# Kernel optimization log

Measured on AMD Instinct MI355X. Metric: run time of the kernel, lower is better.

## Reference

```python
import jax, jax.numpy as jnp
import numpy as np

N_NODES = 120000  # n_entities + n_users
N_REL = 16
D = 64   # entity_dim
R = 64   # relation_dim
E = 1600000


def setup_inputs() -> dict:
    key = jax.random.key(0)
    k1, k2, k3, k4, k5, k6 = jax.random.split(key, 6)
    return {
        "entity_user_embed": jax.random.normal(k1, (N_NODES, D), dtype=jnp.float32) * 0.1,
        "relation_embed": jax.random.normal(k2, (N_REL, R), dtype=jnp.float32) * 0.1,
        "W_R": jax.random.normal(k3, (N_REL, D, R), dtype=jnp.float32) * 0.1,
        "edge_src": jax.random.randint(k4, (E,), 0, N_NODES, dtype=jnp.int32),
        "edge_dst": jax.random.randint(k5, (E,), 0, N_NODES, dtype=jnp.int32),
        "edge_type": jax.random.randint(k6, (E,), 0, N_REL, dtype=jnp.int32),
    }


def reference(entity_user_embed, relation_embed, W_R, edge_src, edge_dst, edge_type):
    n_nodes = entity_user_embed.shape[0]
    # Per-relation transform of every node embedding: [n_rel, n_nodes, R].
    # Equivalent to the per-relation edge loop: matmul(emb[id], W_R[r]).
    trans = jnp.einsum('nd,rdk->rnk', entity_user_embed, W_R)
    r_mul_t = trans[edge_type, edge_src]   # [E, R] (edges.src path)
    r_mul_h = trans[edge_type, edge_dst]   # [E, R] (edges.dst path)
    r_embed = relation_embed[edge_type]    # [E, R]
    # bmm([E,1,R], [E,R,1]) -> per-edge dot product
    att = jnp.sum(r_mul_t * jnp.tanh(r_mul_h + r_embed), axis=-1)  # [E]
    # edge softmax over incoming edges of each destination node
    att_max = jax.ops.segment_max(att, edge_dst, num_segments=n_nodes)
    ex = jnp.exp(att - att_max[edge_dst])
    denom = jax.ops.segment_sum(ex, edge_dst, num_segments=n_nodes)
    out = ex / denom[edge_dst]
    return out[:, None]  # [E, 1], matching squeeze(-1) of [E,1,1]
```

## Files before the change

kernel.cpp:

```cpp
#include <hip/hip_runtime.h>
#include <hip/hip_bf16.h>

#define D64 64
#define NREL 16
#define SCALE 32.0f
#define INV_SCALE 0.03125f

typedef __attribute__((ext_vector_type(8))) short bf16x8;
typedef __attribute__((ext_vector_type(4))) float f32x4;
typedef __attribute__((ext_vector_type(2))) float f32x2;

__device__ __forceinline__ float tanh_fast(float x) {
    float e = __expf(2.0f * x);
    return 1.0f - 2.0f / (e + 1.0f);
}

__device__ __forceinline__ float tanh_poly(float x) {
    x = fmaxf(-1.5f, fminf(1.5f, x));
    float u = x * x;
    float p = fmaf(u, -0.0182227f, 0.108952f);
    p = fmaf(u, p, -0.329139f);
    p = fmaf(u, p, 1.0f);
    return x * p;
}

__device__ __forceinline__ unsigned short f2b(float x) {
    __hip_bfloat16 h = __float2bfloat16(x);
    return *reinterpret_cast<unsigned short*>(&h);
}

__global__ void prep_kernel(const float* __restrict__ WR, const float* __restrict__ rel,
                            unsigned short* __restrict__ Wt, float* __restrict__ relp,
                            float* __restrict__ denom, int n_nodes) {
    int i = blockIdx.x * blockDim.x + threadIdx.x;
    if (i < NREL * D64 * D64) {
        int r = i >> 12, rem = i & 4095, c = rem >> 6, d = rem & 63;
        Wt[i] = f2b(WR[(r << 12) + (d << 6) + c] * SCALE);
    }
    if (i < NREL * D64) {
        int t = i >> 6, kp = i & 63;
        int q = kp >> 4, m = (kp >> 2) & 3, g = kp & 3;
        relp[i] = rel[t * D64 + m * 16 + q * 4 + g];
    }
    if (i < n_nodes) denom[i] = 0.0f;
}

__global__ __launch_bounds__(256)
void trans_gemm_kernel(const float* __restrict__ emb,
                       const unsigned short* __restrict__ Wt,
                       uint4* __restrict__ trans,
                       int n_nodes) {
    __shared__ unsigned short lbuf[8 * 4096];
    const int tid  = threadIdx.x;
    const int lane = tid & 63;
    const int wid  = tid >> 6;
    const int col  = lane & 15;
    const int quad = lane >> 4;
    const int rbase = (blockIdx.x & 1) * 8;
    const int nodebase = (blockIdx.x >> 1) * 256 + wid * 64;

    const unsigned short* wbase = Wt + (rbase << 12);
    #pragma unroll
    for (int k = 0; k < 16; ++k) {
        int c = tid + k * 256;
        int rr = c >> 9, cc = c & 511;
        int mt = cc >> 7, q2 = (cc >> 6) & 1, ln = cc & 63;
        int so = (rr << 12) + ((mt * 16 + (ln & 15)) << 6) + (q2 << 5) + ((ln >> 4) << 3);
        *(bf16x8*)(&lbuf[c << 3]) = *(const bf16x8*)(wbase + so);
    }

    bf16x8 bfr[4][2];
    int nds[4];
    #pragma unroll
    for (int j = 0; j < 4; ++j) {
        int node = nodebase + j * 16 + col;
        nds[j] = node;
        int cn = node < n_nodes ? node : n_nodes - 1;
        const float* bp = emb + (size_t)cn * D64 + quad * 8;
        #pragma unroll
        for (int ks = 0; ks < 2; ++ks) {
            float4 v0 = *(const float4*)(bp + ks * 32);
            float4 v1 = *(const float4*)(bp + ks * 32 + 4);
            bfr[j][ks][0] = (short)f2b(v0.x); bfr[j][ks][1] = (short)f2b(v0.y);
            bfr[j][ks][2] = (short)f2b(v0.z); bfr[j][ks][3] = (short)f2b(v0.w);
            bfr[j][ks][4] = (short)f2b(v1.x); bfr[j][ks][5] = (short)f2b(v1.y);
            bfr[j][ks][6] = (short)f2b(v1.z); bfr[j][ks][7] = (short)f2b(v1.w);
        }
    }

    __syncthreads();

    #pragma unroll 1
    for (int rr = 0; rr < 8; ++rr) {
        const int r = rbase + rr;
        const unsigned short* lb = lbuf + (rr << 12);
        f32x4 acc[4][4];
        #pragma unroll
        for (int mt = 0; mt < 4; ++mt) {
            bf16x8 a0 = *(const bf16x8*)(lb + (mt << 10) + (lane << 3));
            bf16x8 a1 = *(const bf16x8*)(lb + (mt << 10) + 512 + (lane << 3));
            #pragma unroll
            for (int j = 0; j < 4; ++j) {
                f32x4 c = {0.f, 0.f, 0.f, 0.f};
                c = __builtin_amdgcn_mfma_f32_16x16x32_bf16(a0, bfr[j][0], c, 0, 0, 0);
                c = __builtin_amdgcn_mfma_f32_16x16x32_bf16(a1, bfr[j][1], c, 0, 0, 0);
                acc[mt][j] = c;
            }
        }
        #pragma unroll
        for (int j = 0; j < 4; ++j) {
            if (nds[j] < n_nodes) {
                uint4 pk;
                unsigned p;
                p = __builtin_amdgcn_cvt_pk_fp8_f32(acc[0][j][0], acc[0][j][1], 0, false);
                p = __builtin_amdgcn_cvt_pk_fp8_f32(acc[0][j][2], acc[0][j][3], p, true);
                pk.x = p;
                p = __builtin_amdgcn_cvt_pk_fp8_f32(acc[1][j][0], acc[1][j][1], 0, false);
                p = __builtin_amdgcn_cvt_pk_fp8_f32(acc[1][j][2], acc[1][j][3], p, true);
                pk.y = p;
                p = __builtin_amdgcn_cvt_pk_fp8_f32(acc[2][j][0], acc[2][j][1], 0, false);
                p = __builtin_amdgcn_cvt_pk_fp8_f32(acc[2][j][2], acc[2][j][3], p, true);
                pk.z = p;
                p = __builtin_amdgcn_cvt_pk_fp8_f32(acc[3][j][0], acc[3][j][1], 0, false);
                p = __builtin_amdgcn_cvt_pk_fp8_f32(acc[3][j][2], acc[3][j][3], p, true);
                pk.w = p;
                trans[((size_t)r * n_nodes + nds[j]) * 4 + quad] = pk;
            }
        }
    }
}

__device__ __forceinline__ void term4(unsigned ut, unsigned uh, float4 r, float& acc) {
    f32x2 tlo = __builtin_amdgcn_cvt_pk_f32_fp8(ut, false);
    f32x2 thi = __builtin_amdgcn_cvt_pk_f32_fp8(ut, true);
    f32x2 hlo = __builtin_amdgcn_cvt_pk_f32_fp8(uh, false);
    f32x2 hhi = __builtin_amdgcn_cvt_pk_f32_fp8(uh, true);
    acc += tlo[0] * tanh_poly(fmaf(hlo[0], INV_SCALE, r.x));
    acc += tlo[1] * tanh_poly(fmaf(hlo[1], INV_SCALE, r.y));
    acc += thi[0] * tanh_poly(fmaf(hhi[0], INV_SCALE, r.z));
    acc += thi[1] * tanh_poly(fmaf(hhi[1], INV_SCALE, r.w));
}

__global__ __launch_bounds__(256)
void edge_kernel(const unsigned* __restrict__ trans,
                 const float* __restrict__ relp,
                 const int* __restrict__ esrc, const int* __restrict__ edst,
                 const int* __restrict__ etype,
                 float* __restrict__ out, float* __restrict__ denom,
                 int E, int n_nodes) {
    int e0 = blockIdx.x * 512 + threadIdx.x;
    int e1 = e0 + 256;
    bool v0 = e0 < E, v1 = e1 < E;
    int i0 = v0 ? e0 : 0;
    int i1 = v1 ? e1 : 0;
    int t0 = etype[i0], s0 = esrc[i0], d0 = edst[i0];
    int t1 = etype[i1], s1 = esrc[i1], d1 = edst[i1];

    const uint4* pt0 = (const uint4*)(trans + ((size_t)t0 * n_nodes + s0) * 16);
    const uint4* ph0 = (const uint4*)(trans + ((size_t)t0 * n_nodes + d0) * 16);
    const uint4* pt1 = (const uint4*)(trans + ((size_t)t1 * n_nodes + s1) * 16);
    const uint4* ph1 = (const uint4*)(trans + ((size_t)t1 * n_nodes + d1) * 16);

    uint4 T0[4], H0[4], T1[4], H1[4];
    #pragma unroll
    for (int c4 = 0; c4 < 4; ++c4) {
        T0[c4] = pt0[c4]; H0[c4] = ph0[c4];
        T1[c4] = pt1[c4]; H1[c4] = ph1[c4];
    }

    const float4* pr0 = (const float4*)(relp + t0 * D64);
    const float4* pr1 = (const float4*)(relp + t1 * D64);
    float a0 = 0.f, a1 = 0.f;
    #pragma unroll
    for (int c4 = 0; c4 < 4; ++c4) {
        term4(T0[c4].x, H0[c4].x, pr0[c4 * 4 + 0], a0);
        term4(T1[c4].x, H1[c4].x, pr1[c4 * 4 + 0], a1);
        term4(T0[c4].y, H0[c4].y, pr0[c4 * 4 + 1], a0);
        term4(T1[c4].y, H1[c4].y, pr1[c4 * 4 + 1], a1);
        term4(T0[c4].z, H0[c4].z, pr0[c4 * 4 + 2], a0);
        term4(T1[c4].z, H1[c4].z, pr1[c4 * 4 + 2], a1);
        term4(T0[c4].w, H0[c4].w, pr0[c4 * 4 + 3], a0);
        term4(T1[c4].w, H1[c4].w, pr1[c4 * 4 + 3], a1);
    }
    if (v0) {
        float ex = __expf(a0 * INV_SCALE);
        out[e0] = ex;
        atomicAdd(&denom[d0], ex);
    }
    if (v1) {
        float ex = __expf(a1 * INV_SCALE);
        out[e1] = ex;
        atomicAdd(&denom[d1], ex);
    }
}

__global__ void normalize_kernel(float* __restrict__ out,
                                 const float* __restrict__ denom,
                                 const int* __restrict__ edst, int E) {
    int e = blockIdx.x * blockDim.x + threadIdx.x;
    if (e < E) out[e] = out[e] / denom[edst[e]];
}

__global__ void zero_denom_kernel(float* __restrict__ denom, int n) {
    int i = blockIdx.x * blockDim.x + threadIdx.x;
    if (i < n) denom[i] = 0.0f;
}

__global__ __launch_bounds__(256)
void edge_att_fallback(const float* __restrict__ emb, const float* __restrict__ rel,
                       const float* __restrict__ WR, const int* __restrict__ esrc,
                       const int* __restrict__ edst, const int* __restrict__ etype,
                       float* __restrict__ exbuf, float* __restrict__ denom,
                       int E, int chunkSize) {
    const int type = blockIdx.x & 15;
    const int c    = blockIdx.x >> 4;
    const int lane = threadIdx.x & 63;
    const int wid  = threadIdx.x >> 6;
    long base0 = (long)c * (long)chunkSize;
    long cend  = base0 + chunkSize;
    if (cend > E) cend = E;
    if (base0 >= cend) return;
    int per = (chunkSize + 3) >> 2;
    long wbeg = base0 + (long)wid * per;
    long wend = wbeg + per;
    if (wend > cend) wend = cend;
    if (wbeg >= wend) return;
    float w[D64];
    const float* Wt = WR + (size_t)type * D64 * D64;
    #pragma unroll
    for (int d = 0; d < D64; ++d) w[d] = Wt[d * D64 + lane];
    const float rk = rel[type * D64 + lane];
    for (long s0 = wbeg; s0 < wend; s0 += 64) {
        long e = s0 + lane;
        int ty = -1, sv = 0, dv = 0;
        if (e < wend) { ty = etype[e]; sv = esrc[e]; dv = edst[e]; }
        unsigned long long m = __ballot(ty == type);
        while (m) {
            int b = __builtin_ctzll(m);
            m &= m - 1;
            int sn = __builtin_amdgcn_readlane(sv, b);
            int dn = __builtin_amdgcn_readlane(dv, b);
            const float4* es4 = (const float4*)(emb + (size_t)sn * D64);
            const float4* ed4 = (const float4*)(emb + (size_t)dn * D64);
            float t0 = 0.f, t1 = 0.f, t2 = 0.f, t3 = 0.f;
            float h0 = 0.f, h1 = 0.f, h2 = 0.f, h3 = 0.f;
            #pragma unroll
            for (int i = 0; i < D64 / 4; ++i) {
                float4 a = es4[i]; float4 b4 = ed4[i];
                t0 = fmaf(a.x, w[4*i+0], t0); t1 = fmaf(a.y, w[4*i+1], t1);
                t2 = fmaf(a.z, w[4*i+2], t2); t3 = fmaf(a.w, w[4*i+3], t3);
                h0 = fmaf(b4.x, w[4*i+0], h0); h1 = fmaf(b4.y, w[4*i+1], h1);
                h2 = fmaf(b4.z, w[4*i+2], h2); h3 = fmaf(b4.w, w[4*i+3], h3);
            }
            float t = (t0 + t1) + (t2 + t3);
            float h = (h0 + h1) + (h2 + h3);
            float p = t * tanh_fast(h + rk);
            #pragma unroll
            for (int off = 32; off > 0; off >>= 1) p += __shfl_xor(p, off);
            if (lane == 0) {
                float ex = __expf(p);
                exbuf[s0 + b] = ex;
                atomicAdd(&denom[dn], ex);
            }
        }
    }
}

__global__ void normalize_fallback(float* __restrict__ out,
                                   const float* __restrict__ denom,
                                   const int* __restrict__ edst, int E) {
    int e = blockIdx.x * blockDim.x + threadIdx.x;
    if (e < E) out[e] = out[e] / denom[edst[e]];
}

extern "C" void kernel_launch(void* const* d_in, const int* in_sizes, int n_in,
                              void* d_out, int out_size, void* d_ws, size_t ws_size,
                              hipStream_t stream) {
    const float* emb  = (const float*)d_in[0];
    const float* rel  = (const float*)d_in[1];
    const float* WR   = (const float*)d_in[2];
    const int*   esrc = (const int*)d_in[3];
    const int*   edst = (const int*)d_in[4];
    const int*   ety  = (const int*)d_in[5];

    const int E       = in_sizes[3];
    const int n_nodes = in_sizes[0] / D64;
    float* out = (float*)d_out;

    size_t transB = (size_t)NREL * n_nodes * D64;
    size_t off_trans = 0;
    size_t off_wt    = (off_trans + transB + 255) & ~(size_t)255;
    size_t off_rel   = (off_wt + (size_t)NREL * D64 * D64 * 2 + 255) & ~(size_t)255;
    size_t off_den   = (off_rel + (size_t)NREL * D64 * 4 + 255) & ~(size_t)255;
    size_t need      = off_den + (size_t)n_nodes * sizeof(float);

    if (ws_size >= need) {
        uint4*          trans = (uint4*)((char*)d_ws + off_trans);
        unsigned short* Wt    = (unsigned short*)((char*)d_ws + off_wt);
        float*          relp  = (float*)((char*)d_ws + off_rel);
        float*          denom = (float*)((char*)d_ws + off_den);

        int prepN = n_nodes > NREL * D64 * D64 ? n_nodes : NREL * D64 * D64;
        prep_kernel<<<(prepN + 255) / 256, 256, 0, stream>>>(WR, rel, Wt, relp,
                                                             denom, n_nodes);
        trans_gemm_kernel<<<((n_nodes + 255) / 256) * 2, 256, 0, stream>>>(emb, Wt, trans, n_nodes);
        edge_kernel<<<(E + 511) / 512, 256, 0, stream>>>((const unsigned*)trans, relp,
                                                         esrc, edst, ety,
                                                         out, denom, E, n_nodes);
        normalize_kernel<<<(E + 255) / 256, 256, 0, stream>>>(out, denom, edst, E);
    } else {
        float* denom = (float*)d_ws;
        zero_denom_kernel<<<(n_nodes + 255) / 256, 256, 0, stream>>>(denom, n_nodes);
        const int NCHUNK = 256;
        int chunk = (E + NCHUNK - 1) / NCHUNK;
        edge_att_fallback<<<16 * NCHUNK, 256, 0, stream>>>(emb, rel, WR, esrc, edst, ety,
                                                           out, denom, E, chunk);
        normalize_fallback<<<(E + 255) / 256, 256, 0, stream>>>(out, denom, edst, E);
    }
}
```

Measured before the change: 241.3 us.

## Fuse edge attention and normalization into one cooperative kernel with grid sync

Replaces the separate edge and normalize kernels with a persistent cooperative kernel that computes exp-scores and accumulates the denominators, keeps the scores and destination ids in shared memory, does a grid-wide sync, and then normalizes. This removes one kernel launch and the global write/read of out and edst between the two passes. In exchange it caps the grid at 512 blocks, uses 32 KB of LDS per block, which may reduce occupancy, and adds grid-sync overhead. The old two-kernel path is kept as a fallback if the cooperative launch fails.

```diff
diff --git a/kernel.cpp b/kernel.cpp
--- a/kernel.cpp
+++ b/kernel.cpp
@@ -1,10 +1,15 @@
 #include <hip/hip_runtime.h>
 #include <hip/hip_bf16.h>
+#include <hip/hip_cooperative_groups.h>
+
+namespace cg = cooperative_groups;
 
 #define D64 64
 #define NREL 16
 #define SCALE 32.0f
 #define INV_SCALE 0.03125f
+#define FBLK 512
+#define MAXE 16
 
 typedef __attribute__((ext_vector_type(8))) short bf16x8;
 typedef __attribute__((ext_vector_type(4))) float f32x4;
@@ -141,6 +146,63 @@
     acc += thi[1] * tanh_poly(fmaf(hhi[1], INV_SCALE, r.w));
 }
 
+__device__ __forceinline__ float edge_att_val(const unsigned* __restrict__ trans,
+                                              const float* __restrict__ relp,
+                                              int t, int s, int d, int n_nodes) {
+    const uint4*  pt = (const uint4*)(trans + ((size_t)t * n_nodes + s) * 16);
+    const uint4*  ph = (const uint4*)(trans + ((size_t)t * n_nodes + d) * 16);
+    const float4* pr = (const float4*)(relp + t * D64);
+    float acc = 0.f;
+    #pragma unroll
+    for (int c4 = 0; c4 < 4; ++c4) {
+        uint4 ut = pt[c4];
+        uint4 uh = ph[c4];
+        term4(ut.x, uh.x, pr[c4 * 4 + 0], acc);
+        term4(ut.y, uh.y, pr[c4 * 4 + 1], acc);
+        term4(ut.z, uh.z, pr[c4 * 4 + 2], acc);
+        term4(ut.w, uh.w, pr[c4 * 4 + 3], acc);
+    }
+    return __expf(acc * INV_SCALE);
+}
+
+__global__ __launch_bounds__(256, 2)
+void fused_edge_kernel(const unsigned* __restrict__ trans,
+                       const float* __restrict__ relp,
+                       const int* __restrict__ esrc, const int* __restrict__ edst,
+                       const int* __restrict__ etype,
+                       float* __restrict__ out, float* __restrict__ denom,
+                       int E, int n_nodes, int ept) {
+    __shared__ float exv[MAXE * 256];
+    __shared__ int   ddv[MAXE * 256];
+    cg::grid_group grid = cg::this_grid();
+    const int tid = threadIdx.x;
+    const int stride = FBLK * 256;
+    const int base = blockIdx.x * 256 + tid;
+
+    #pragma unroll 1
+    for (int k = 0; k < ept; ++k) {
+        int e = base + k * stride;
+        float ex = 0.f;
+        int d = 0;
+        if (e < E) {
+            int t = etype[e], s = esrc[e];
+            d = edst[e];
+            ex = edge_att_val(trans, relp, t, s, d, n_nodes);
+            atomicAdd(&denom[d], ex);
+        }
+        exv[k * 256 + tid] = ex;
+        ddv[k * 256 + tid] = d;
+    }
+
+    grid.sync();
+
+    #pragma unroll 1
+    for (int k = 0; k < ept; ++k) {
+        int e = base + k * stride;
+        if (e < E) out[e] = exv[k * 256 + tid] / denom[ddv[k * 256 + tid]];
+    }
+}
+
 __global__ __launch_bounds__(256)
 void edge_kernel(const unsigned* __restrict__ trans,
                  const float* __restrict__ relp,
@@ -155,43 +217,10 @@
     int i1 = v1 ? e1 : 0;
     int t0 = etype[i0], s0 = esrc[i0], d0 = edst[i0];
     int t1 = etype[i1], s1 = esrc[i1], d1 = edst[i1];
-
-    const uint4* pt0 = (const uint4*)(trans + ((size_t)t0 * n_nodes + s0) * 16);
-    const uint4* ph0 = (const uint4*)(trans + ((size_t)t0 * n_nodes + d0) * 16);
-    const uint4* pt1 = (const uint4*)(trans + ((size_t)t1 * n_nodes + s1) * 16);
-    const uint4* ph1 = (const uint4*)(trans + ((size_t)t1 * n_nodes + d1) * 16);
-
-    uint4 T0[4], H0[4], T1[4], H1[4];
-    #pragma unroll
-    for (int c4 = 0; c4 < 4; ++c4) {
-        T0[c4] = pt0[c4]; H0[c4] = ph0[c4];
-        T1[c4] = pt1[c4]; H1[c4] = ph1[c4];
-    }
-
-    const float4* pr0 = (const float4*)(relp + t0 * D64);
-    const float4* pr1 = (const float4*)(relp + t1 * D64);
-    float a0 = 0.f, a1 = 0.f;
-    #pragma unroll
-    for (int c4 = 0; c4 < 4; ++c4) {
-        term4(T0[c4].x, H0[c4].x, pr0[c4 * 4 + 0], a0);
-        term4(T1[c4].x, H1[c4].x, pr1[c4 * 4 + 0], a1);
-        term4(T0[c4].y, H0[c4].y, pr0[c4 * 4 + 1], a0);
-        term4(T1[c4].y, H1[c4].y, pr1[c4 * 4 + 1], a1);
-        term4(T0[c4].z, H0[c4].z, pr0[c4 * 4 + 2], a0);
-        term4(T1[c4].z, H1[c4].z, pr1[c4 * 4 + 2], a1);
-        term4(T0[c4].w, H0[c4].w, pr0[c4 * 4 + 3], a0);
-        term4(T1[c4].w, H1[c4].w, pr1[c4 * 4 + 3], a1);
-    }
-    if (v0) {
-        float ex = __expf(a0 * INV_SCALE);
-        out[e0] = ex;
-        atomicAdd(&denom[d0], ex);
-    }
-    if (v1) {
-        float ex = __expf(a1 * INV_SCALE);
-        out[e1] = ex;
-        atomicAdd(&denom[d1], ex);
-    }
+    float ex0 = edge_att_val(trans, relp, t0, s0, d0, n_nodes);
+    float ex1 = edge_att_val(trans, relp, t1, s1, d1, n_nodes);
+    if (v0) { out[e0] = ex0; atomicAdd(&denom[d0], ex0); }
+    if (v1) { out[e1] = ex1; atomicAdd(&denom[d1], ex1); }
 }
 
 __global__ void normalize_kernel(float* __restrict__ out,
@@ -304,10 +333,24 @@
         prep_kernel<<<(prepN + 255) / 256, 256, 0, stream>>>(WR, rel, Wt, relp,
                                                              denom, n_nodes);
         trans_gemm_kernel<<<((n_nodes + 255) / 256) * 2, 256, 0, stream>>>(emb, Wt, trans, n_nodes);
-        edge_kernel<<<(E + 511) / 512, 256, 0, stream>>>((const unsigned*)trans, relp,
-                                                         esrc, edst, ety,
-                                                         out, denom, E, n_nodes);
-        normalize_kernel<<<(E + 255) / 256, 256, 0, stream>>>(out, denom, edst, E);
+
+        const unsigned* transU = (const unsigned*)trans;
+        int ept = (E + FBLK * 256 - 1) / (FBLK * 256);
+        bool coop_ok = (ept <= MAXE);
+        if (coop_ok) {
+            void* args[] = {(void*)&transU, (void*)&relp, (void*)&esrc, (void*)&edst,
+                            (void*)&ety, (void*)&out, (void*)&denom,
+                            (void*)&E, (void*)&n_nodes, (void*)&ept};
+            hipError_t err = hipLaunchCooperativeKernel(
+                (const void*)fused_edge_kernel, dim3(FBLK), dim3(256), args, 0, stream);
+            coop_ok = (err == hipSuccess);
+        }
+        if (!coop_ok) {
+            edge_kernel<<<(E + 511) / 512, 256, 0, stream>>>(transU, relp,
+                                                             esrc, edst, ety,
+                                                             out, denom, E, n_nodes);
+            normalize_kernel<<<(E + 255) / 256, 256, 0, stream>>>(out, denom, edst, E);
+        }
     } else {
         float* denom = (float*)d_ws;
         zero_denom_kernel<<<(n_nodes + 255) / 256, 256, 0, stream>>>(denom, n_nodes);
```

Result: slower. 327.8 us (+35.9%).
